# Kernel optimization log

Measured on AMD Instinct MI355X. Metric: run time of the kernel, lower is better.

## Reference

```python
import jax, jax.numpy as jnp
import numpy as np

N, IN_DIM, HID, HEADS, HOPS, NCLS, E = 20000, 1536, 256, 4, 3, 3, 320000
HD = HID // HEADS
EPS = 1e-5
NEG_SLOPE = 0.2


def layer_norm(x, g, b):
    mu = jnp.mean(x, axis=-1, keepdims=True)
    var = jnp.var(x, axis=-1, keepdims=True)
    return (x - mu) * jax.lax.rsqrt(var + EPS) * g + b


def gatv2(x, src, dst, Wl, bl, Wr, br, att, bias):
    # x: [N, HID]; src/dst: [E'] (self loops included)
    xl = (x @ Wl + bl).reshape(N, HEADS, HD)  # source transform
    xr = (x @ Wr + br).reshape(N, HEADS, HD)  # target transform
    e = jax.nn.leaky_relu(xl[src] + xr[dst], NEG_SLOPE)          # [E', H, D]
    logits = jnp.einsum('ehd,hd->eh', e, att)                     # [E', H]
    m = jax.ops.segment_max(logits, dst, num_segments=N)         # [N, H]
    ex = jnp.exp(logits - m[dst])
    denom = jax.ops.segment_sum(ex, dst, num_segments=N)
    alpha = ex / denom[dst]                                       # softmax per dst
    msg = xl[src] * alpha[:, :, None]                             # [E', H, D]
    out = jax.ops.segment_sum(msg, dst, num_segments=N)
    return out.reshape(N, HID) + bias


def setup_inputs() -> dict:
    key = jax.random.key(0)
    ks = jax.random.split(key, 20)
    s = lambda k, shp, sc: jax.random.normal(k, shp, jnp.float32) * sc
    return {
        'features': s(ks[0], (N, IN_DIM), 1.0),
        'edge_index': jax.random.randint(ks[1], (2, E), 0, N, jnp.int64),
        'proj_W': s(ks[2], (IN_DIM, HID), 0.02),
        'proj_b': jnp.zeros((HID,), jnp.float32),
        'n0_g': jnp.ones((HID,), jnp.float32),
        'n0_b': jnp.zeros((HID,), jnp.float32),
        'Wl': s(ks[3], (HOPS, HID, HID), 0.05),
        'bl': jnp.zeros((HOPS, HID), jnp.float32),
        'Wr': s(ks[4], (HOPS, HID, HID), 0.05),
        'br': jnp.zeros((HOPS, HID), jnp.float32),
        'att': s(ks[5], (HOPS, HEADS, HD), 0.1),
        'gbias': jnp.zeros((HOPS, HID), jnp.float32),
        'ln_g': jnp.ones((HOPS, HID), jnp.float32),
        'ln_b': jnp.zeros((HOPS, HID), jnp.float32),
        'h1_W': s(ks[6], (HID, HID), 0.05),
        'h1_b': jnp.zeros((HID,), jnp.float32),
        'h2_W': s(ks[7], (HID, NCLS), 0.05),
        'h2_b': jnp.zeros((NCLS,), jnp.float32),
    }


def reference(features, edge_index, proj_W, proj_b, n0_g, n0_b, Wl, bl, Wr, br,
              att, gbias, ln_g, ln_b, h1_W, h1_b, h2_W, h2_b):
    # add self loops (PyG GATv2Conv default)
    loop = jnp.arange(N, dtype=edge_index.dtype)
    src = jnp.concatenate([edge_index[0], loop])
    dst = jnp.concatenate([edge_index[1], loop])

    x = layer_norm(features @ proj_W + proj_b, n0_g, n0_b)
    for h in range(HOPS):
        g = gatv2(x, src, dst, Wl[h], bl[h], Wr[h], br[h], att[h], gbias[h])
        x = layer_norm(g + x, ln_g[h], ln_b[h])
    # head (dropout inactive at eval); torch GELU is exact erf form
    x = jax.nn.gelu(x @ h1_W + h1_b, approximate=False)
    return x @ h2_W + h2_b
```

## Files before the change

kernel.cpp:

```cpp
#include <hip/hip_runtime.h>
#include <hip/hip_bf16.h>
#include <math.h>

#define NN 20000
#define INDIM 1536
#define HID 256
#define NE 320000
#define NEDGE (NE + NN)
#define EPSV 1e-5f
#define NEG 0.2f

typedef unsigned short ushort_b;
typedef unsigned int uint32;
typedef __bf16 bf16x8 __attribute__((ext_vector_type(8)));
typedef float f32x4 __attribute__((ext_vector_type(4)));

#define AS1(p) ((const __attribute__((address_space(1))) void*)(p))
#define AS3(p) ((__attribute__((address_space(3))) void*)(p))

__device__ inline ushort_b f2bf(float x) {
  union { float f; uint32 u; } v; v.f = x;
  uint32 r = v.u + 0x7FFFu + ((v.u >> 16) & 1u);
  return (ushort_b)(r >> 16);
}
__device__ inline float bf2f(ushort_b h) {
  union { uint32 u; float f; } v; v.u = ((uint32)h) << 16;
  return v.f;
}
__device__ inline float4 ldbf4(const ushort_b* p) {
  ushort4 u = *(const ushort4*)p;
  float4 f;
  f.x = bf2f(u.x); f.y = bf2f(u.y); f.z = bf2f(u.z); f.w = bf2f(u.w);
  return f;
}

template<int OUTMODE>
__global__ __launch_bounds__(256, 3) void gemm_mfma(
    const float* __restrict__ Af,
    const ushort_b* __restrict__ Bt0, const ushort_b* __restrict__ Bt1,
    const float* __restrict__ bias0, const float* __restrict__ bias1,
    void* __restrict__ C0, void* __restrict__ C1,
    int Mstore, int Kloop, int Kstride, int kb0, int kb1, int loOff)
{
  __shared__ ushort_b As0h[64 * 32], As0l[64 * 32], As1h[64 * 32], As1l[64 * 32];
  __shared__ ushort_b Bs0h[128 * 32], Bs0l[128 * 32], Bs1h[128 * 32], Bs1l[128 * 32];
  const ushort_b* Bt = blockIdx.z ? Bt1 : Bt0;
  const float* bias  = blockIdx.z ? bias1 : bias0;
  void* Cv           = blockIdx.z ? C1 : C0;
  int kbase          = blockIdx.z ? kb1 : kb0;

  int tid = threadIdx.x;
  int wave = tid >> 6, lane = tid & 63;
  int r0 = blockIdx.y * 64;
  int c0 = blockIdx.x * 128;
  int wn = wave << 5;
  int mrow = lane & 15, quad = lane >> 4;
  int nk = Kloop >> 5;
  size_t loB = (size_t)loOff * 2;

  f32x4 acc[4][2] = {};
  float4 pA0[2], pA1[2];

  auto issueB = [&](int k0, ushort_b* ldsH, ushort_b* ldsL) {
#pragma unroll
    for (int it = 0; it < 2; it++) {
      int off = (wave << 10) + (it << 12) + (lane << 4);
      int row = off >> 6, colb = off & 63;
      const char* g = (const char*)Bt + ((size_t)(c0 + row) * Kstride + kbase + k0) * 2 + colb;
      __builtin_amdgcn_global_load_lds(AS1(g), AS3((char*)ldsH + off), 16, 0, 0);
      __builtin_amdgcn_global_load_lds(AS1(g + loB), AS3((char*)ldsL + off), 16, 0, 0);
    }
  };
  auto loadA = [&](int k0, float4* dst) {
#pragma unroll
    for (int p = 0; p < 2; p++) {
      int off4 = (p << 8) + tid;
      int row = off4 >> 3, col4 = off4 & 7;
      int grow = r0 + row;
      dst[p] = (grow < Mstore)
          ? *(const float4*)(Af + (size_t)grow * Kstride + kbase + k0 + (col4 << 2))
          : make_float4(0.f, 0.f, 0.f, 0.f);
    }
  };
  auto writeA = [&](const float4* src, ushort_b* ldsH, ushort_b* ldsL) {
#pragma unroll
    for (int p = 0; p < 2; p++) {
      int off4 = (p << 8) + tid;
      int row = off4 >> 3, col4 = off4 & 7;
      ushort_b h0 = f2bf(src[p].x), h1 = f2bf(src[p].y);
      ushort_b h2 = f2bf(src[p].z), h3 = f2bf(src[p].w);
      uint2 uh;
      uh.x = (uint32)h0 | ((uint32)h1 << 16);
      uh.y = (uint32)h2 | ((uint32)h3 << 16);
      uint2 ul;
      ul.x = (uint32)f2bf(src[p].x - bf2f(h0)) | ((uint32)f2bf(src[p].y - bf2f(h1)) << 16);
      ul.y = (uint32)f2bf(src[p].z - bf2f(h2)) | ((uint32)f2bf(src[p].w - bf2f(h3)) << 16);
      *(uint2*)(ldsH + (row << 5) + (col4 << 2)) = uh;
      *(uint2*)(ldsL + (row << 5) + (col4 << 2)) = ul;
    }
  };
  auto computeStage = [&](const ushort_b* AsH, const ushort_b* AsL,
                          const ushort_b* BsH, const ushort_b* BsL) {
    bf16x8 ah[4], al[4], bh[2], bl[2];
#pragma unroll
    for (int t = 0; t < 4; t++) {
      int o = (((t << 4) + mrow) << 5) + (quad << 3);
      ah[t] = *(const bf16x8*)(AsH + o);
      al[t] = *(const bf16x8*)(AsL + o);
    }
#pragma unroll
    for (int u = 0; u < 2; u++) {
      int o = ((wn + (u << 4) + mrow) << 5) + (quad << 3);
      bh[u] = *(const bf16x8*)(BsH + o);
      bl[u] = *(const bf16x8*)(BsL + o);
    }
#pragma unroll
    for (int t = 0; t < 4; t++)
#pragma unroll
      for (int u = 0; u < 2; u++) {
        acc[t][u] = __builtin_amdgcn_mfma_f32_16x16x32_bf16(ah[t], bh[u], acc[t][u], 0, 0, 0);
        acc[t][u] = __builtin_amdgcn_mfma_f32_16x16x32_bf16(al[t], bh[u], acc[t][u], 0, 0, 0);
        acc[t][u] = __builtin_amdgcn_mfma_f32_16x16x32_bf16(ah[t], bl[u], acc[t][u], 0, 0, 0);
      }
  };

  loadA(0, pA0);
  issueB(0, Bs0h, Bs0l);
  loadA(32, pA1);
  writeA(pA0, As0h, As0l);

  for (int k = 0; k < nk; k += 2) {
    __syncthreads();
    if (k + 1 < nk) {
      issueB((k + 1) << 5, Bs1h, Bs1l);
      writeA(pA1, As1h, As1l);
      if (k + 2 < nk) loadA((k + 2) << 5, pA0);
    }
    computeStage(As0h, As0l, Bs0h, Bs0l);
    __syncthreads();
    if (k + 2 < nk) {
      issueB((k + 2) << 5, Bs0h, Bs0l);
      writeA(pA0, As0h, As0l);
      if (k + 3 < nk) loadA((k + 3) << 5, pA1);
    }
    computeStage(As1h, As1l, Bs1h, Bs1l);
  }

#pragma unroll
  for (int u = 0; u < 2; u++) {
    int col = c0 + wn + (u << 4) + mrow;
    float bb = bias[col];
#pragma unroll
    for (int t = 0; t < 4; t++) {
#pragma unroll
      for (int r = 0; r < 4; r++) {
        int row = r0 + (t << 4) + (quad << 2) + r;
        if (row < Mstore) {
          float v = acc[t][u][r] + bb;
          if (OUTMODE == 3) v = 0.5f * v * (1.f + erff(v * 0.70710678118654752f));
          if (OUTMODE == 2) ((ushort_b*)Cv)[(size_t)row * 256 + col] = f2bf(v);
          else              ((float*)Cv)[(size_t)row * 256 + col] = v;
        }
      }
    }
  }
}

__global__ __launch_bounds__(256) void transpose_cast(
    const float* __restrict__ in, ushort_b* __restrict__ out, int R, int C)
{
  __shared__ float t[32][33];
  int bx = blockIdx.x * 32;
  int by = blockIdx.y * 32;
  for (int i = threadIdx.y; i < 32; i += 8)
    t[i][threadIdx.x] = in[(size_t)(by + i) * C + bx + threadIdx.x];
  __syncthreads();
  size_t plane = (size_t)R * C;
  for (int i = threadIdx.y; i < 32; i += 8) {
    float v = t[threadIdx.x][i];
    ushort_b h = f2bf(v);
    size_t o = (size_t)(bx + i) * R + by + threadIdx.x;
    out[o] = h;
    out[plane + o] = f2bf(v - bf2f(h));
  }
}

__global__ __launch_bounds__(256) void transpose7(
    const float* __restrict__ Wl, const float* __restrict__ Wr,
    const float* __restrict__ h1W, ushort_b* __restrict__ dst_base)
{
  int z = blockIdx.z;
  const float* in = (z < 3) ? Wl + (size_t)z * 65536
                  : (z < 6) ? Wr + (size_t)(z - 3) * 65536
                            : h1W;
  ushort_b* out = dst_base + (size_t)z * 65536;
  __shared__ float t[32][33];
  int bx = blockIdx.x * 32;
  int by = blockIdx.y * 32;
  for (int i = threadIdx.y; i < 32; i += 8)
    t[i][threadIdx.x] = in[(size_t)(by + i) * 256 + bx + threadIdx.x];
  __syncthreads();
  for (int i = threadIdx.y; i < 32; i += 8) {
    float v = t[threadIdx.x][i];
    ushort_b h = f2bf(v);
    size_t o = (size_t)(bx + i) * 256 + by + threadIdx.x;
    out[o] = h;
    out[(size_t)7 * 65536 + o] = f2bf(v - bf2f(h));
  }
}

__global__ __launch_bounds__(256) void ln_sum_kernel(
    const float* __restrict__ in0, const float* __restrict__ in1,
    const float* __restrict__ g, const float* __restrict__ b,
    float* __restrict__ out, int n)
{
  int wave = threadIdx.x >> 6, lane = threadIdx.x & 63;
  int row = blockIdx.x * 4 + wave;
  if (row >= n) return;
  int c = lane << 2;
  float4 v = *(const float4*)(in0 + (size_t)row * HID + c);
  float4 v1 = *(const float4*)(in1 + (size_t)row * HID + c);
  v.x += v1.x; v.y += v1.y; v.z += v1.z; v.w += v1.w;
  float s1 = v.x + v.y + v.z + v.w;
  float s2 = v.x * v.x + v.y * v.y + v.z * v.z + v.w * v.w;
#pragma unroll
  for (int m = 1; m < 64; m <<= 1) {
    s1 += __shfl_xor(s1, m, 64);
    s2 += __shfl_xor(s2, m, 64);
  }
  float mu = s1 * (1.f / 256.f);
  float var = s2 * (1.f / 256.f) - mu * mu;
  float rstd = rsqrtf(var + EPSV);
  float4 gv = *(const float4*)(g + c);
  float4 bv = *(const float4*)(b + c);
  float4 o;
  o.x = (v.x - mu) * rstd * gv.x + bv.x;
  o.y = (v.y - mu) * rstd * gv.y + bv.y;
  o.z = (v.z - mu) * rstd * gv.z + bv.z;
  o.w = (v.w - mu) * rstd * gv.w + bv.w;
  *(float4*)(out + (size_t)row * HID + c) = o;
}

__global__ void count_kernel(const int* __restrict__ ei, int* __restrict__ cnt)
{
  int e = blockIdx.x * blockDim.x + threadIdx.x;
  if (e < NEDGE) {
    int d = (e < NE) ? ei[NE + e] : (e - NE);
    atomicAdd(&cnt[d], 1);
  }
}

__global__ __launch_bounds__(1024) void scan_kernel(
    const int* __restrict__ cnt, int* __restrict__ offs, int* __restrict__ cursor)
{
  __shared__ int sums[1024];
  int tid = threadIdx.x;
  const int CH = 20;
  int base = tid * CH;
  int loc[CH];
  int s = 0;
#pragma unroll
  for (int i = 0; i < CH; i++) {
    int idx = base + i;
    int v = (idx < NN) ? cnt[idx] : 0;
    loc[i] = s;
    s += v;
  }
  sums[tid] = s;
  __syncthreads();
  for (int off = 1; off < 1024; off <<= 1) {
    int t = (tid >= off) ? sums[tid - off] : 0;
    __syncthreads();
    sums[tid] += t;
    __syncthreads();
  }
  int pre = (tid == 0) ? 0 : sums[tid - 1];
#pragma unroll
  for (int i = 0; i < CH; i++) {
    int idx = base + i;
    if (idx < NN) { int e = pre + loc[i]; offs[idx] = e; cursor[idx] = e; }
  }
  if (tid == 0) offs[NN] = NEDGE;
}

__global__ void scatter_kernel(const int* __restrict__ ei, int* __restrict__ cursor,
                               int* __restrict__ csr_src)
{
  int e = blockIdx.x * blockDim.x + threadIdx.x;
  if (e < NEDGE) {
    int s, d;
    if (e < NE) { s = ei[e]; d = ei[NE + e]; }
    else { s = e - NE; d = e - NE; }
    int p = atomicAdd(&cursor[d], 1);
    csr_src[p] = s;
  }
}

__device__ inline float edge_logit(float4 xv, float4 xrv, float4 attv) {
  float e0 = xv.x + xrv.x, e1 = xv.y + xrv.y, e2 = xv.z + xrv.z, e3 = xv.w + xrv.w;
  e0 = (e0 > 0.f) ? e0 : NEG * e0;
  e1 = (e1 > 0.f) ? e1 : NEG * e1;
  e2 = (e2 > 0.f) ? e2 : NEG * e2;
  e3 = (e3 > 0.f) ? e3 : NEG * e3;
  float lc = e0 * attv.x + e1 * attv.y + e2 * attv.z + e3 * attv.w;
  lc += __shfl_xor(lc, 1, 16);
  lc += __shfl_xor(lc, 2, 16);
  lc += __shfl_xor(lc, 4, 16);
  lc += __shfl_xor(lc, 8, 16);
  return lc;
}

#define ACCUM(i, lg, xv) {                          \
    float w = __expf(lg);                            \
    lS[i] += w;                                      \
    pS##i##0 += w * xv.x; pS##i##1 += w * xv.y;      \
    pS##i##2 += w * xv.z; pS##i##3 += w * xv.w; }

__global__ __launch_bounds__(256) void gat_kernel(
    const ushort_b* __restrict__ xl, const ushort_b* __restrict__ xr,
    const float* __restrict__ x_in, const float* __restrict__ att,
    const float* __restrict__ gbias, const float* __restrict__ ln_g,
    const float* __restrict__ ln_b, const int* __restrict__ offs,
    const int* __restrict__ csr_src, float* __restrict__ x_out)
{
  __shared__ float gbuf[2][64][5];
  int wave = threadIdx.x >> 6, lane = threadIdx.x & 63;
  int nib = wave >> 1, sub = wave & 1;
  int node = blockIdx.x * 2 + nib;
  int c = lane << 2;
  float4 xrv = ldbf4(xr + (size_t)node * HID + c);
  float4 attv = *(const float4*)(att + c);

  float lS[4] = {0.f, 0.f, 0.f, 0.f};
  float pS00 = 0.f, pS01 = 0.f, pS02 = 0.f, pS03 = 0.f;
  float pS10 = 0.f, pS11 = 0.f, pS12 = 0.f, pS13 = 0.f;
  float pS20 = 0.f, pS21 = 0.f, pS22 = 0.f, pS23 = 0.f;
  float pS30 = 0.f, pS31 = 0.f, pS32 = 0.f, pS33 = 0.f;

  int beg = offs[node], end = offs[node + 1];
  int mid = beg + ((end - beg + 1) >> 1);
  int e  = sub ? mid : beg;
  int e1 = sub ? end : mid;
  for (; e + 3 < e1; e += 4) {
    int s0 = csr_src[e], s1 = csr_src[e + 1], s2 = csr_src[e + 2], s3 = csr_src[e + 3];
    float4 x0v = ldbf4(xl + (size_t)s0 * HID + c);
    float4 x1v = ldbf4(xl + (size_t)s1 * HID + c);
    float4 x2v = ldbf4(xl + (size_t)s2 * HID + c);
    float4 x3v = ldbf4(xl + (size_t)s3 * HID + c);
    float g0 = edge_logit(x0v, xrv, attv);
    float g1 = edge_logit(x1v, xrv, attv);
    float g2 = edge_logit(x2v, xrv, attv);
    float g3 = edge_logit(x3v, xrv, attv);
    ACCUM(0, g0, x0v);
    ACCUM(1, g1, x1v);
    ACCUM(2, g2, x2v);
    ACCUM(3, g3, x3v);
  }
  for (; e < e1; e++) {
    int s0 = csr_src[e];
    float4 x0v = ldbf4(xl + (size_t)s0 * HID + c);
    float g0 = edge_logit(x0v, xrv, attv);
    ACCUM(0, g0, x0v);
  }

  float l  = lS[0] + lS[1] + lS[2] + lS[3];
  float q0 = pS00 + pS10 + pS20 + pS30;
  float q1 = pS01 + pS11 + pS21 + pS31;
  float q2 = pS02 + pS12 + pS22 + pS32;
  float q3 = pS03 + pS13 + pS23 + pS33;

  if (sub) {
    gbuf[nib][lane][0] = l;
    gbuf[nib][lane][1] = q0;
    gbuf[nib][lane][2] = q1;
    gbuf[nib][lane][3] = q2;
    gbuf[nib][lane][4] = q3;
  }
  __syncthreads();
  if (sub) return;

  l  += gbuf[nib][lane][0];
  q0 += gbuf[nib][lane][1];
  q1 += gbuf[nib][lane][2];
  q2 += gbuf[nib][lane][3];
  q3 += gbuf[nib][lane][4];

  float inv = 1.f / l;
  float4 xv = *(const float4*)(x_in + (size_t)node * HID + c);
  float4 gb = *(const float4*)(gbias + c);
  float o0 = q0 * inv + gb.x + xv.x;
  float o1 = q1 * inv + gb.y + xv.y;
  float o2 = q2 * inv + gb.z + xv.z;
  float o3 = q3 * inv + gb.w + xv.w;
  float s1s = o0 + o1 + o2 + o3;
  float s2s = o0 * o0 + o1 * o1 + o2 * o2 + o3 * o3;
#pragma unroll
  for (int mmk = 1; mmk < 64; mmk <<= 1) {
    s1s += __shfl_xor(s1s, mmk, 64);
    s2s += __shfl_xor(s2s, mmk, 64);
  }
  float mu = s1s * (1.f / 256.f);
  float var = s2s * (1.f / 256.f) - mu * mu;
  float rstd = rsqrtf(var + EPSV);
  float4 gv = *(const float4*)(ln_g + c);
  float4 bv = *(const float4*)(ln_b + c);
  float4 o;
  o.x = (o0 - mu) * rstd * gv.x + bv.x;
  o.y = (o1 - mu) * rstd * gv.y + bv.y;
  o.z = (o2 - mu) * rstd * gv.z + bv.z;
  o.w = (o3 - mu) * rstd * gv.w + bv.w;
  *(float4*)(x_out + (size_t)node * HID + c) = o;
}

__global__ __launch_bounds__(256) void head2_kernel(
    const float* __restrict__ t1, const float* __restrict__ W,
    const float* __restrict__ bias, float* __restrict__ out)
{
  int wave = threadIdx.x >> 6, lane = threadIdx.x & 63;
  int row = blockIdx.x * 4 + wave;
  if (row >= NN) return;
  int c = lane << 2;
  float4 v = *(const float4*)(t1 + (size_t)row * HID + c);
  float p0 = 0.f, p1 = 0.f, p2 = 0.f;
#pragma unroll
  for (int j = 0; j < 4; j++) {
    float vj = (&v.x)[j];
    p0 += vj * W[(c + j) * 3 + 0];
    p1 += vj * W[(c + j) * 3 + 1];
    p2 += vj * W[(c + j) * 3 + 2];
  }
#pragma unroll
  for (int mm = 1; mm < 64; mm <<= 1) {
    p0 += __shfl_xor(p0, mm, 64);
    p1 += __shfl_xor(p1, mm, 64);
    p2 += __shfl_xor(p2, mm, 64);
  }
  if (lane == 0) {
    out[(size_t)row * 3 + 0] = p0 + bias[0];
    out[(size_t)row * 3 + 1] = p1 + bias[1];
    out[(size_t)row * 3 + 2] = p2 + bias[2];
  }
}

extern "C" void kernel_launch(void* const* d_in, const int* in_sizes, int n_in,
                              void* d_out, int out_size, void* d_ws, size_t ws_size,
                              hipStream_t stream)
{
  const float* features = (const float*)d_in[0];
  const int*   ei       = (const int*)d_in[1];
  const float* proj_W   = (const float*)d_in[2];
  const float* proj_b   = (const float*)d_in[3];
  const float* n0_g     = (const float*)d_in[4];
  const float* n0_b     = (const float*)d_in[5];
  const float* Wl       = (const float*)d_in[6];
  const float* bl       = (const float*)d_in[7];
  const float* Wr       = (const float*)d_in[8];
  const float* br       = (const float*)d_in[9];
  const float* att      = (const float*)d_in[10];
  const float* gbias    = (const float*)d_in[11];
  const float* ln_g     = (const float*)d_in[12];
  const float* ln_b     = (const float*)d_in[13];
  const float* h1_W     = (const float*)d_in[14];
  const float* h1_b     = (const float*)d_in[15];
  const float* h2_W     = (const float*)d_in[16];
  const float* h2_b     = (const float*)d_in[17];
  float* out = (float*)d_out;

  char* w = (char*)d_ws;
  float*    x0    = (float*)w;    w += (size_t)NN * HID * 4;
  float*    x1    = (float*)w;    w += (size_t)NN * HID * 4;
  float*    part1 = (float*)w;    w += (size_t)NN * HID * 4;
  ushort_b* xlb   = (ushort_b*)w; w += (size_t)NN * HID * 2;
  ushort_b* xrb   = (ushort_b*)w; w += (size_t)NN * HID * 2;
  ushort_b* wtp   = (ushort_b*)w; w += (size_t)2 * HID * INDIM * 2;
  ushort_b* w7    = (ushort_b*)w; w += (size_t)14 * HID * HID * 2;
  float* zbias = (float*)w; w += (size_t)HID * 4;
  int* cnt     = (int*)w;  w += (size_t)NN * 4;
  int* offs    = (int*)w;  w += (size_t)(NN + 1) * 4;
  int* cursor  = (int*)w;  w += (size_t)NN * 4;
  int* csr     = (int*)w;  w += (size_t)NEDGE * 4;

  hipMemsetAsync(cnt, 0, (size_t)NN * 4, stream);
  hipMemsetAsync(zbias, 0, (size_t)HID * 4, stream);
  count_kernel<<<(NEDGE + 255) / 256, 256, 0, stream>>>(ei, cnt);
  scan_kernel<<<1, 1024, 0, stream>>>(cnt, offs, cursor);
  scatter_kernel<<<(NEDGE + 255) / 256, 256, 0, stream>>>(ei, cursor, csr);

  transpose_cast<<<dim3(HID / 32, INDIM / 32), dim3(32, 8), 0, stream>>>(proj_W, wtp, INDIM, HID);
  transpose7<<<dim3(8, 8, 7), dim3(32, 8), 0, stream>>>(Wl, Wr, h1_W, w7);

  const int MB = (NN + 63) / 64;
  dim3 gsplit(2, MB, 2);
  dim3 gsingle(2, MB, 1);

  const int loP = HID * INDIM;
  const int lo7 = 7 * HID * HID;

  gemm_mfma<0><<<gsplit, 256, 0, stream>>>(
      features, wtp, wtp, proj_b, zbias, x1, part1, NN, INDIM / 2, INDIM, 0, INDIM / 2, loP);
  ln_sum_kernel<<<(NN + 3) / 4, 256, 0, stream>>>(x1, part1, n0_g, n0_b, x0, NN);

  float* xcur = x0;
  float* xnxt = x1;
  for (int h = 0; h < 3; h++) {
    gemm_mfma<2><<<gsplit, 256, 0, stream>>>(
        xcur, w7 + (size_t)h * HID * HID, w7 + (size_t)(3 + h) * HID * HID,
        bl + h * HID, br + h * HID, xlb, xrb, NN, HID, HID, 0, 0, lo7);
    gat_kernel<<<NN / 2, 256, 0, stream>>>(
        xlb, xrb, xcur, att + h * HID, gbias + h * HID,
        ln_g + h * HID, ln_b + h * HID, offs, csr, xnxt);
    float* t = xcur; xcur = xnxt; xnxt = t;
  }

  gemm_mfma<3><<<gsingle, 256, 0, stream>>>(
      xcur, w7 + (size_t)6 * HID * HID, w7 + (size_t)6 * HID * HID,
      h1_b, h1_b, part1, part1, NN, HID, HID, 0, 0, lo7);
  head2_kernel<<<(NN + 3) / 4, 256, 0, stream>>>(part1, h2_W, h2_b, out);
}
```

Baseline: 627.8 us.

## Triple-buffer B tiles with manual waitcnt barriers in split-bf16 GEMM

Moves the MFMA GEMM's B-tile pipeline from double to triple buffering in LDS, so B loads are issued two stages ahead. The __syncthreads are replaced by explicit s_waitcnt vmcnt counts plus s_barrier, so outstanding global loads can keep flowing across the barrier. Out-of-range A rows are clamped instead of branched, which gives a uniform load count for the vmcnt accounting. The extra LDS lowers occupancy from 3 to 2 blocks per CU, and the hand-written vmcnt values are fragile if the compiler reorders or merges loads.

```diff
diff --git a/kernel.cpp b/kernel.cpp
--- a/kernel.cpp
+++ b/kernel.cpp
@@ -35,7 +35,7 @@
 }
 
 template<int OUTMODE>
-__global__ __launch_bounds__(256, 3) void gemm_mfma(
+__global__ __launch_bounds__(256, 2) void gemm_mfma(
     const float* __restrict__ Af,
     const ushort_b* __restrict__ Bt0, const ushort_b* __restrict__ Bt1,
     const float* __restrict__ bias0, const float* __restrict__ bias1,
@@ -43,7 +43,9 @@
     int Mstore, int Kloop, int Kstride, int kb0, int kb1, int loOff)
 {
   __shared__ ushort_b As0h[64 * 32], As0l[64 * 32], As1h[64 * 32], As1l[64 * 32];
-  __shared__ ushort_b Bs0h[128 * 32], Bs0l[128 * 32], Bs1h[128 * 32], Bs1l[128 * 32];
+  __shared__ ushort_b Bs0h[128 * 32], Bs0l[128 * 32];
+  __shared__ ushort_b Bs1h[128 * 32], Bs1l[128 * 32];
+  __shared__ ushort_b Bs2h[128 * 32], Bs2l[128 * 32];
   const ushort_b* Bt = blockIdx.z ? Bt1 : Bt0;
   const float* bias  = blockIdx.z ? bias1 : bias0;
   void* Cv           = blockIdx.z ? C1 : C0;
@@ -59,7 +61,7 @@
   size_t loB = (size_t)loOff * 2;
 
   f32x4 acc[4][2] = {};
-  float4 pA0[2], pA1[2];
+  float4 pAa[2], pAb[2];
 
   auto issueB = [&](int k0, ushort_b* ldsH, ushort_b* ldsL) {
 #pragma unroll
@@ -77,9 +79,8 @@
       int off4 = (p << 8) + tid;
       int row = off4 >> 3, col4 = off4 & 7;
       int grow = r0 + row;
-      dst[p] = (grow < Mstore)
-          ? *(const float4*)(Af + (size_t)grow * Kstride + kbase + k0 + (col4 << 2))
-          : make_float4(0.f, 0.f, 0.f, 0.f);
+      if (grow >= Mstore) grow = Mstore - 1;
+      dst[p] = *(const float4*)(Af + (size_t)grow * Kstride + kbase + k0 + (col4 << 2));
     }
   };
   auto writeA = [&](const float4* src, ushort_b* ldsH, ushort_b* ldsL) {
@@ -124,26 +125,45 @@
       }
   };
 
-  loadA(0, pA0);
+  loadA(0, pAa);
   issueB(0, Bs0h, Bs0l);
-  loadA(32, pA1);
-  writeA(pA0, As0h, As0l);
+  loadA(32, pAb);
+  issueB(32, Bs1h, Bs1l);
+  writeA(pAa, As0h, As0l);
+  loadA(64, pAa);
+  asm volatile("s_waitcnt vmcnt(8) lgkmcnt(0)" ::: "memory");
+  __builtin_amdgcn_sched_barrier(0);
+  __builtin_amdgcn_s_barrier();
+  __builtin_amdgcn_sched_barrier(0);
+
+  ushort_b *B0h = Bs0h, *B0l = Bs0l, *B1h = Bs1h, *B1l = Bs1l, *B2h = Bs2h, *B2l = Bs2l;
 
   for (int k = 0; k < nk; k += 2) {
-    __syncthreads();
-    if (k + 1 < nk) {
-      issueB((k + 1) << 5, Bs1h, Bs1l);
-      writeA(pA1, As1h, As1l);
-      if (k + 2 < nk) loadA((k + 2) << 5, pA0);
-    }
-    computeStage(As0h, As0l, Bs0h, Bs0l);
-    __syncthreads();
-    if (k + 2 < nk) {
-      issueB((k + 2) << 5, Bs0h, Bs0l);
-      writeA(pA0, As0h, As0l);
-      if (k + 3 < nk) loadA((k + 3) << 5, pA1);
-    }
-    computeStage(As1h, As1l, Bs1h, Bs1l);
+    if (k + 2 < nk) issueB((k + 2) << 5, B2h, B2l);
+    if (k + 1 < nk) writeA(pAb, As1h, As1l);
+    if (k + 3 < nk) loadA((k + 3) << 5, pAb);
+    computeStage(As0h, As0l, B0h, B0l);
+    if (k + 3 < nk)      { asm volatile("s_waitcnt vmcnt(6) lgkmcnt(0)" ::: "memory"); }
+    else if (k + 2 < nk) { asm volatile("s_waitcnt vmcnt(4) lgkmcnt(0)" ::: "memory"); }
+    else                 { asm volatile("s_waitcnt vmcnt(0) lgkmcnt(0)" ::: "memory"); }
+    __builtin_amdgcn_sched_barrier(0);
+    __builtin_amdgcn_s_barrier();
+    __builtin_amdgcn_sched_barrier(0);
+
+    int k1 = k + 1;
+    if (k1 + 2 < nk) issueB((k1 + 2) << 5, B0h, B0l);
+    if (k1 + 1 < nk) writeA(pAa, As0h, As0l);
+    if (k1 + 3 < nk) loadA((k1 + 3) << 5, pAa);
+    computeStage(As1h, As1l, B1h, B1l);
+    if (k1 + 3 < nk)      { asm volatile("s_waitcnt vmcnt(6) lgkmcnt(0)" ::: "memory"); }
+    else if (k1 + 2 < nk) { asm volatile("s_waitcnt vmcnt(4) lgkmcnt(0)" ::: "memory"); }
+    else                  { asm volatile("s_waitcnt vmcnt(0) lgkmcnt(0)" ::: "memory"); }
+    __builtin_amdgcn_sched_barrier(0);
+    __builtin_amdgcn_s_barrier();
+    __builtin_amdgcn_sched_barrier(0);
+
+    ushort_b* th = B2h; ushort_b* tl = B2l;
+    B2h = B1h; B2l = B1l; B1h = B0h; B1l = B0l; B0h = th; B0l = tl;
   }
 
 #pragma unroll
```

Result: slower. 643.6 us (+2.5%).

## Prepack weights into MFMA fragment order and load A directly to registers

Applied to the files above, without the earlier changes.

Weights are now prepacked into per-chunk MFMA fragment layout (hi and lo bf16 planes), so B tiles are copied contiguously into LDS and read with linear per-lane loads. Each wave loads its own A rows straight from global memory into registers and converts them to bf16 hi/lo there, so A no longer goes through LDS. The LDS pipeline becomes a triple-buffered ring with explicit vmcnt waits and raw s_barrier in place of __syncthreads. This removes A's LDS traffic and the strided B reads, but each wave now covers 16 rows by 128 columns, so B fragments get less reuse per LDS read, and the hand-written waitcnt counts must match the number of outstanding loads.

```diff
diff --git a/kernel.cpp b/kernel.cpp
--- a/kernel.cpp
+++ b/kernel.cpp
@@ -40,10 +40,9 @@
     const ushort_b* __restrict__ Bt0, const ushort_b* __restrict__ Bt1,
     const float* __restrict__ bias0, const float* __restrict__ bias1,
     void* __restrict__ C0, void* __restrict__ C1,
-    int Mstore, int Kloop, int Kstride, int kb0, int kb1, int loOff)
-{
-  __shared__ ushort_b As0h[64 * 32], As0l[64 * 32], As1h[64 * 32], As1l[64 * 32];
-  __shared__ ushort_b Bs0h[128 * 32], Bs0l[128 * 32], Bs1h[128 * 32], Bs1l[128 * 32];
+    int Mstore, int Kloop, int Kstride, int kb0, int kb1)
+{
+  __shared__ ushort_b Bs[3 * 8192];
   const ushort_b* Bt = blockIdx.z ? Bt1 : Bt0;
   const float* bias  = blockIdx.z ? bias1 : bias0;
   void* Cv           = blockIdx.z ? C1 : C0;
@@ -51,162 +50,156 @@
 
   int tid = threadIdx.x;
   int wave = tid >> 6, lane = tid & 63;
+  int quad = lane >> 4, mrow = lane & 15;
   int r0 = blockIdx.y * 64;
-  int c0 = blockIdx.x * 128;
-  int wn = wave << 5;
-  int mrow = lane & 15, quad = lane >> 4;
+  int p  = blockIdx.x;
   int nk = Kloop >> 5;
-  size_t loB = (size_t)loOff * 2;
-
-  f32x4 acc[4][2] = {};
-  float4 pA0[2], pA1[2];
-
-  auto issueB = [&](int k0, ushort_b* ldsH, ushort_b* ldsL) {
-#pragma unroll
-    for (int it = 0; it < 2; it++) {
-      int off = (wave << 10) + (it << 12) + (lane << 4);
-      int row = off >> 6, colb = off & 63;
-      const char* g = (const char*)Bt + ((size_t)(c0 + row) * Kstride + kbase + k0) * 2 + colb;
-      __builtin_amdgcn_global_load_lds(AS1(g), AS3((char*)ldsH + off), 16, 0, 0);
-      __builtin_amdgcn_global_load_lds(AS1(g + loB), AS3((char*)ldsL + off), 16, 0, 0);
+  int nchunk = Kstride >> 5;
+  int cb = kbase >> 5;
+
+  int arow = r0 + (wave << 4) + mrow;
+  if (arow >= Mstore) arow = Mstore - 1;
+  const float* Aptr = Af + (size_t)arow * Kstride + kbase + (quad << 3);
+
+  f32x4 acc[8] = {};
+  float pA0[8], pA1[8];
+
+  auto issueB = [&](int kc, int buf) {
+    const char* g = (const char*)Bt + (((size_t)(p * nchunk + (cb + kc))) << 14);
+    char* l = (char*)Bs + buf * 16384;
+    int o = tid << 4;
+#pragma unroll
+    for (int pl = 0; pl < 2; pl++) {
+      int off = (pl << 13) + o;
+      __builtin_amdgcn_global_load_lds(AS1(g + off), AS3(l + off), 16, 0, 0);
+      __builtin_amdgcn_global_load_lds(AS1(g + off + 4096), AS3(l + off + 4096), 16, 0, 0);
     }
   };
-  auto loadA = [&](int k0, float4* dst) {
-#pragma unroll
-    for (int p = 0; p < 2; p++) {
-      int off4 = (p << 8) + tid;
-      int row = off4 >> 3, col4 = off4 & 7;
-      int grow = r0 + row;
-      dst[p] = (grow < Mstore)
-          ? *(const float4*)(Af + (size_t)grow * Kstride + kbase + k0 + (col4 << 2))
-          : make_float4(0.f, 0.f, 0.f, 0.f);
-    }
+  auto loadA = [&](int k, float* dst) {
+    const float* s = Aptr + (k << 5);
+    *(float4*)(dst)     = *(const float4*)(s);
+    *(float4*)(dst + 4) = *(const float4*)(s + 4);
   };
-  auto writeA = [&](const float4* src, ushort_b* ldsH, ushort_b* ldsL) {
-#pragma unroll
-    for (int p = 0; p < 2; p++) {
-      int off4 = (p << 8) + tid;
-      int row = off4 >> 3, col4 = off4 & 7;
-      ushort_b h0 = f2bf(src[p].x), h1 = f2bf(src[p].y);
-      ushort_b h2 = f2bf(src[p].z), h3 = f2bf(src[p].w);
-      uint2 uh;
-      uh.x = (uint32)h0 | ((uint32)h1 << 16);
-      uh.y = (uint32)h2 | ((uint32)h3 << 16);
-      uint2 ul;
-      ul.x = (uint32)f2bf(src[p].x - bf2f(h0)) | ((uint32)f2bf(src[p].y - bf2f(h1)) << 16);
-      ul.y = (uint32)f2bf(src[p].z - bf2f(h2)) | ((uint32)f2bf(src[p].w - bf2f(h3)) << 16);
-      *(uint2*)(ldsH + (row << 5) + (col4 << 2)) = uh;
-      *(uint2*)(ldsL + (row << 5) + (col4 << 2)) = ul;
-    }
+  auto cvtA = [&](const float* s, bf16x8& hh, bf16x8& ll) {
+    union { bf16x8 v; uint32 u[4]; } H, L;
+#pragma unroll
+    for (int q2 = 0; q2 < 4; q2++) {
+      float a = s[2 * q2], b = s[2 * q2 + 1];
+      ushort_b h0 = f2bf(a), h1 = f2bf(b);
+      H.u[q2] = (uint32)h0 | ((uint32)h1 << 16);
+      L.u[q2] = (uint32)f2bf(a - bf2f(h0)) | ((uint32)f2bf(b - bf2f(h1)) << 16);
+    }
+    hh = H.v; ll = L.v;
   };
-  auto computeStage = [&](const ushort_b* AsH, const ushort_b* AsL,
-                          const ushort_b* BsH, const ushort_b* BsL) {
-    bf16x8 ah[4], al[4], bh[2], bl[2];
-#pragma unroll
-    for (int t = 0; t < 4; t++) {
-      int o = (((t << 4) + mrow) << 5) + (quad << 3);
-      ah[t] = *(const bf16x8*)(AsH + o);
-      al[t] = *(const bf16x8*)(AsL + o);
-    }
-#pragma unroll
-    for (int u = 0; u < 2; u++) {
-      int o = ((wn + (u << 4) + mrow) << 5) + (quad << 3);
-      bh[u] = *(const bf16x8*)(BsH + o);
-      bl[u] = *(const bf16x8*)(BsL + o);
-    }
-#pragma unroll
-    for (int t = 0; t < 4; t++)
-#pragma unroll
-      for (int u = 0; u < 2; u++) {
-        acc[t][u] = __builtin_amdgcn_mfma_f32_16x16x32_bf16(ah[t], bh[u], acc[t][u], 0, 0, 0);
-        acc[t][u] = __builtin_amdgcn_mfma_f32_16x16x32_bf16(al[t], bh[u], acc[t][u], 0, 0, 0);
-        acc[t][u] = __builtin_amdgcn_mfma_f32_16x16x32_bf16(ah[t], bl[u], acc[t][u], 0, 0, 0);
+  auto computeStage = [&](int buf, const bf16x8& ah, const bf16x8& al) {
+    const ushort_b* bp = Bs + buf * 8192;
+#pragma unroll
+    for (int u = 0; u < 8; u++) {
+      bf16x8 bh = *(const bf16x8*)(bp + (u << 9) + (lane << 3));
+      bf16x8 bl = *(const bf16x8*)(bp + 4096 + (u << 9) + (lane << 3));
+      acc[u] = __builtin_amdgcn_mfma_f32_16x16x32_bf16(ah, bh, acc[u], 0, 0, 0);
+      acc[u] = __builtin_amdgcn_mfma_f32_16x16x32_bf16(al, bh, acc[u], 0, 0, 0);
+      acc[u] = __builtin_amdgcn_mfma_f32_16x16x32_bf16(ah, bl, acc[u], 0, 0, 0);
+    }
+  };
+
+  loadA(0, pA0);
+  issueB(0, 0);
+  issueB(1, 1);
+  loadA(1, pA1);
+  asm volatile("s_waitcnt vmcnt(6)" ::: "memory");
+  __builtin_amdgcn_sched_barrier(0);
+  __builtin_amdgcn_s_barrier();
+  __builtin_amdgcn_sched_barrier(0);
+
+  int bcur = 0;
+  for (int k = 0; k < nk; k += 2) {
+    int b1 = bcur + 1; if (b1 >= 3) b1 -= 3;
+    int b2 = bcur + 2; if (b2 >= 3) b2 -= 3;
+
+    {
+      bf16x8 ah, al;
+      cvtA(pA0, ah, al);
+      if (k + 2 < nk) { issueB(k + 2, b2); loadA(k + 2, pA0); }
+      computeStage(bcur, ah, al);
+      if (k + 2 < nk) { asm volatile("s_waitcnt vmcnt(6)" ::: "memory"); }
+      else            { asm volatile("s_waitcnt vmcnt(2)" ::: "memory"); }
+      __builtin_amdgcn_sched_barrier(0);
+      __builtin_amdgcn_s_barrier();
+      __builtin_amdgcn_sched_barrier(0);
+    }
+    {
+      bf16x8 ah, al;
+      cvtA(pA1, ah, al);
+      if (k + 3 < nk) { issueB(k + 3, bcur); loadA(k + 3, pA1); }
+      computeStage(b1, ah, al);
+      if (k + 3 < nk) {
+        asm volatile("s_waitcnt vmcnt(6)" ::: "memory");
+        __builtin_amdgcn_sched_barrier(0);
+        __builtin_amdgcn_s_barrier();
+        __builtin_amdgcn_sched_barrier(0);
       }
-  };
-
-  loadA(0, pA0);
-  issueB(0, Bs0h, Bs0l);
-  loadA(32, pA1);
-  writeA(pA0, As0h, As0l);
-
-  for (int k = 0; k < nk; k += 2) {
-    __syncthreads();
-    if (k + 1 < nk) {
-      issueB((k + 1) << 5, Bs1h, Bs1l);
-      writeA(pA1, As1h, As1l);
-      if (k + 2 < nk) loadA((k + 2) << 5, pA0);
-    }
-    computeStage(As0h, As0l, Bs0h, Bs0l);
-    __syncthreads();
-    if (k + 2 < nk) {
-      issueB((k + 2) << 5, Bs0h, Bs0l);
-      writeA(pA0, As0h, As0l);
-      if (k + 3 < nk) loadA((k + 3) << 5, pA1);
-    }
-    computeStage(As1h, As1l, Bs1h, Bs1l);
-  }
-
-#pragma unroll
-  for (int u = 0; u < 2; u++) {
-    int col = c0 + wn + (u << 4) + mrow;
+    }
+    bcur = b2;
+  }
+
+#pragma unroll
+  for (int u = 0; u < 8; u++) {
+    int col = (p << 7) + (u << 4) + mrow;
     float bb = bias[col];
 #pragma unroll
-    for (int t = 0; t < 4; t++) {
-#pragma unroll
-      for (int r = 0; r < 4; r++) {
-        int row = r0 + (t << 4) + (quad << 2) + r;
-        if (row < Mstore) {
-          float v = acc[t][u][r] + bb;
-          if (OUTMODE == 3) v = 0.5f * v * (1.f + erff(v * 0.70710678118654752f));
-          if (OUTMODE == 2) ((ushort_b*)Cv)[(size_t)row * 256 + col] = f2bf(v);
-          else              ((float*)Cv)[(size_t)row * 256 + col] = v;
-        }
+    for (int r = 0; r < 4; r++) {
+      int row = r0 + (wave << 4) + (quad << 2) + r;
+      if (row < Mstore) {
+        float v = acc[u][r] + bb;
+        if (OUTMODE == 3) v = 0.5f * v * (1.f + erff(v * 0.70710678118654752f));
+        if (OUTMODE == 2) ((ushort_b*)Cv)[(size_t)row * 256 + col] = f2bf(v);
+        else              ((float*)Cv)[(size_t)row * 256 + col] = v;
       }
     }
   }
 }
 
-__global__ __launch_bounds__(256) void transpose_cast(
-    const float* __restrict__ in, ushort_b* __restrict__ out, int R, int C)
-{
-  __shared__ float t[32][33];
-  int bx = blockIdx.x * 32;
-  int by = blockIdx.y * 32;
-  for (int i = threadIdx.y; i < 32; i += 8)
-    t[i][threadIdx.x] = in[(size_t)(by + i) * C + bx + threadIdx.x];
-  __syncthreads();
-  size_t plane = (size_t)R * C;
-  for (int i = threadIdx.y; i < 32; i += 8) {
-    float v = t[threadIdx.x][i];
-    ushort_b h = f2bf(v);
-    size_t o = (size_t)(bx + i) * R + by + threadIdx.x;
-    out[o] = h;
-    out[plane + o] = f2bf(v - bf2f(h));
-  }
-}
-
-__global__ __launch_bounds__(256) void transpose7(
+__device__ inline void prep_body(const float* __restrict__ W, int ldw, int nchunk,
+                                 ushort_b* __restrict__ out, int c, int p, int tid)
+{
+  ushort_b* base = out + (((size_t)(p * nchunk + c)) << 13);
+#pragma unroll
+  for (int g0 = 0; g0 < 2; g0++) {
+    int g = tid + (g0 << 8);
+    int u = g >> 6, l = g & 63;
+    int quad = l >> 4, mrow = l & 15;
+    int col = (p << 7) + (u << 4) + mrow;
+    int krow = (c << 5) + (quad << 3);
+    uint32 hu[4], lu[4];
+#pragma unroll
+    for (int q2 = 0; q2 < 4; q2++) {
+      float a = W[(size_t)(krow + 2 * q2) * ldw + col];
+      float b = W[(size_t)(krow + 2 * q2 + 1) * ldw + col];
+      ushort_b h0 = f2bf(a), h1 = f2bf(b);
+      hu[q2] = (uint32)h0 | ((uint32)h1 << 16);
+      lu[q2] = (uint32)f2bf(a - bf2f(h0)) | ((uint32)f2bf(b - bf2f(h1)) << 16);
+    }
+    *(uint4*)(base + (size_t)g * 8)        = make_uint4(hu[0], hu[1], hu[2], hu[3]);
+    *(uint4*)(base + 4096 + (size_t)g * 8) = make_uint4(lu[0], lu[1], lu[2], lu[3]);
+  }
+}
+
+__global__ __launch_bounds__(256) void prep_frag(
+    const float* __restrict__ W, int ldw, int nchunk, ushort_b* __restrict__ out)
+{
+  prep_body(W, ldw, nchunk, out, blockIdx.x, blockIdx.y, threadIdx.x);
+}
+
+__global__ __launch_bounds__(256) void prep_frag7(
     const float* __restrict__ Wl, const float* __restrict__ Wr,
-    const float* __restrict__ h1W, ushort_b* __restrict__ dst_base)
+    const float* __restrict__ h1W, ushort_b* __restrict__ dst)
 {
   int z = blockIdx.z;
-  const float* in = (z < 3) ? Wl + (size_t)z * 65536
-                  : (z < 6) ? Wr + (size_t)(z - 3) * 65536
-                            : h1W;
-  ushort_b* out = dst_base + (size_t)z * 65536;
-  __shared__ float t[32][33];
-  int bx = blockIdx.x * 32;
-  int by = blockIdx.y * 32;
-  for (int i = threadIdx.y; i < 32; i += 8)
-    t[i][threadIdx.x] = in[(size_t)(by + i) * 256 + bx + threadIdx.x];
-  __syncthreads();
-  for (int i = threadIdx.y; i < 32; i += 8) {
-    float v = t[threadIdx.x][i];
-    ushort_b h = f2bf(v);
-    size_t o = (size_t)(bx + i) * 256 + by + threadIdx.x;
-    out[o] = h;
-    out[(size_t)7 * 65536 + o] = f2bf(v - bf2f(h));
-  }
+  const float* W = (z < 3) ? Wl + (size_t)z * 65536
+                 : (z < 6) ? Wr + (size_t)(z - 3) * 65536
+                           : h1W;
+  prep_body(W, 256, 8, dst + (size_t)z * 131072, blockIdx.x, blockIdx.y, threadIdx.x);
 }
 
 __global__ __launch_bounds__(256) void ln_sum_kernel(
@@ -486,26 +479,23 @@
   scan_kernel<<<1, 1024, 0, stream>>>(cnt, offs, cursor);
   scatter_kernel<<<(NEDGE + 255) / 256, 256, 0, stream>>>(ei, cursor, csr);
 
-  transpose_cast<<<dim3(HID / 32, INDIM / 32), dim3(32, 8), 0, stream>>>(proj_W, wtp, INDIM, HID);
-  transpose7<<<dim3(8, 8, 7), dim3(32, 8), 0, stream>>>(Wl, Wr, h1_W, w7);
+  prep_frag<<<dim3(INDIM / 32, 2), 256, 0, stream>>>(proj_W, HID, INDIM / 32, wtp);
+  prep_frag7<<<dim3(8, 2, 7), 256, 0, stream>>>(Wl, Wr, h1_W, w7);
 
   const int MB = (NN + 63) / 64;
   dim3 gsplit(2, MB, 2);
   dim3 gsingle(2, MB, 1);
 
-  const int loP = HID * INDIM;
-  const int lo7 = 7 * HID * HID;
-
   gemm_mfma<0><<<gsplit, 256, 0, stream>>>(
-      features, wtp, wtp, proj_b, zbias, x1, part1, NN, INDIM / 2, INDIM, 0, INDIM / 2, loP);
+      features, wtp, wtp, proj_b, zbias, x1, part1, NN, INDIM / 2, INDIM, 0, INDIM / 2);
   ln_sum_kernel<<<(NN + 3) / 4, 256, 0, stream>>>(x1, part1, n0_g, n0_b, x0, NN);
 
   float* xcur = x0;
   float* xnxt = x1;
   for (int h = 0; h < 3; h++) {
     gemm_mfma<2><<<gsplit, 256, 0, stream>>>(
-        xcur, w7 + (size_t)h * HID * HID, w7 + (size_t)(3 + h) * HID * HID,
-        bl + h * HID, br + h * HID, xlb, xrb, NN, HID, HID, 0, 0, lo7);
+        xcur, w7 + (size_t)h * 131072, w7 + (size_t)(3 + h) * 131072,
+        bl + h * HID, br + h * HID, xlb, xrb, NN, HID, HID, 0, 0);
     gat_kernel<<<NN / 2, 256, 0, stream>>>(
         xlb, xrb, xcur, att + h * HID, gbias + h * HID,
         ln_g + h * HID, ln_b + h * HID, offs, csr, xnxt);
@@ -513,7 +503,7 @@
   }
 
   gemm_mfma<3><<<gsingle, 256, 0, stream>>>(
-      xcur, w7 + (size_t)6 * HID * HID, w7 + (size_t)6 * HID * HID,
-      h1_b, h1_b, part1, part1, NN, HID, HID, 0, 0, lo7);
+      xcur, w7 + (size_t)6 * 131072, w7 + (size_t)6 * 131072,
+      h1_b, h1_b, part1, part1, NN, HID, HID, 0, 0);
   head2_kernel<<<(NN + 3) / 4, 256, 0, stream>>>(part1, h2_W, h2_b, out);
 }
```

New measurement: 591.0 us. -5.9%, faster.
